# Optimization experiments

Measured on AMD Instinct MI355X. Metric: run time of the kernel, lower is better.

The kernel has to match this reference:

```python
import jax, jax.numpy as jnp
import numpy as np

NUM_LAYERS = 2
H = 1024
B = 16
L = 2048


def setup_inputs() -> dict:
    key = jax.random.key(0)
    ks = jax.random.split(key, 14)
    s = 1.0 / np.sqrt(H)
    inp = {"x": jax.random.normal(ks[0], (B, L, H), dtype=jnp.float32)}
    names = ["Wf", "Uf", "Wi", "Ui", "Wo", "Uo", "Wc", "Uc"]
    for j, n in enumerate(names):
        inp[n] = jax.random.uniform(ks[1 + j], (NUM_LAYERS, H, H), dtype=jnp.float32, minval=-s, maxval=s)
    for j, n in enumerate(["bf", "bi", "bo", "bc"]):
        inp[n] = jax.random.uniform(ks[9 + j], (NUM_LAYERS, H), dtype=jnp.float32, minval=-s, maxval=s)
    return inp


def _lstm_layer(x, W4, U4, b4, h0, c0):
    # x: [B,L,H]; W4,U4: [4H,H] packed as (f,i,o,c); b4: [4H]
    xg = jnp.einsum("blh,gh->blg", x, W4)  # [B,L,4H] input projections, one big GEMM
    xg = jnp.swapaxes(xg, 0, 1)  # [L,B,4H]

    def step(carry, xg_t):
        h, c = carry
        g = xg_t + h @ U4.T + b4  # [B,4H]
        f, i, o, cc = jnp.split(g, 4, axis=-1)
        f = jax.nn.sigmoid(f)
        i = jax.nn.sigmoid(i)
        o = jax.nn.sigmoid(o)
        c = f * c + i * jnp.tanh(cc)
        h = o * jnp.tanh(c)
        return (h, c), h

    (h_t, c_t), hs = jax.lax.scan(step, (h0, c0), xg)
    return jnp.swapaxes(hs, 0, 1), (h_t, c_t)  # [B,L,H]


def _forward(x, Wf, Uf, bf, Wi, Ui, bi, Wo, Uo, bo, Wc, Uc, bc):
    b, l, h = x.shape
    state = None
    for layer in range(NUM_LAYERS):
        W4 = jnp.concatenate([Wf[layer], Wi[layer], Wo[layer], Wc[layer]], axis=0)
        U4 = jnp.concatenate([Uf[layer], Ui[layer], Uo[layer], Uc[layer]], axis=0)
        b4 = jnp.concatenate([bf[layer], bi[layer], bo[layer], bc[layer]], axis=0)
        if state is None:
            h0 = jnp.zeros((b, h), dtype=x.dtype)
            c0 = jnp.zeros((b, h), dtype=x.dtype)
        else:
            h0, c0 = state  # source passes previous layer's final state onward
        x, state = _lstm_layer(x, W4, U4, b4, h0, c0)
        # dropout is identity in eval mode
    return x


def reference(x, Wf, Uf, bf, Wi, Ui, bi, Wo, Uo, bo, Wc, Uc, bc):
    return _forward(x, Wf, Uf, bf, Wi, Ui, bi, Wo, Uo, bo, Wc, Uc, bc)
```

## Files before the change

kernel.cpp:

```cpp
#include <hip/hip_runtime.h>


typedef _Float16 half8 __attribute__((ext_vector_type(8)));
typedef float    float4v __attribute__((ext_vector_type(4)));
typedef unsigned long long u64;

#define NBLK 256
#define NTHR 512
#define BB   16
#define LL   2048
#define HH   1024
#define KK   2048
#define NJ   4
#define NR   16
#define NSTEP 4096

#define WS_XT16   0u
#define WS_H1SEQ  67108864u
#define WS_HCUR   134217728u
#define WS_FLAGS  134283264u

struct ScanParams {
  const float* W[4];
  const float* U[4];
  const float* bias4[4];
  const _Float16* xT;
  _Float16* h1seq;
  _Float16* hcur;
  float* dout;
  unsigned* flags;
};

__global__ void prep_convert(const float* __restrict__ x, _Float16* __restrict__ xT) {
  size_t id = (size_t)blockIdx.x * blockDim.x + threadIdx.x;
  int k8 = (int)(id & (HH / 8 - 1)) * 8;
  size_t bt = id >> 7;
  int b = (int)(bt >> 11);
  int t = (int)(bt & (LL - 1));
  const float* src = x + (bt << 10) + k8;
  float4v v0 = *(const float4v*)(src);
  float4v v1 = *(const float4v*)(src + 4);
  half8 o;
  o[0] = (_Float16)v0[0]; o[1] = (_Float16)v0[1]; o[2] = (_Float16)v0[2]; o[3] = (_Float16)v0[3];
  o[4] = (_Float16)v1[0]; o[5] = (_Float16)v1[1]; o[6] = (_Float16)v1[2]; o[7] = (_Float16)v1[3];
  *(half8*)(xT + (((size_t)t * BB + b) << 10) + k8) = o;
}

__global__ void prep_init(_Float16* hcur, unsigned* flags) {
  int i = blockIdx.x * blockDim.x + threadIdx.x;
  if (i < 2 * BB * HH) hcur[i] = (_Float16)0.f;
  if (i < 1024) flags[i] = 0u;
}

__device__ __forceinline__ float sigm(float x) { return 1.f / (1.f + __expf(-x)); }
__device__ __forceinline__ float tanh_fast(float x) { return 1.f - 2.f / (1.f + __expf(2.f * x)); }

__global__ __launch_bounds__(NTHR, 2) void lstm_scan(ScanParams p) {
  __shared__ _Float16 wlds[2][NR][KK];
  __shared__ float acc_s[8][16][17];
  __shared__ float g_s[16][17];
  __shared__ float bias_s[2][NR];

  const int tid  = threadIdx.x;
  const int blk  = blockIdx.x;
  const int wv   = tid >> 6;
  const int lane = tid & 63;
  const int frow = lane & 15;
  const int kgrp = lane >> 4;

  for (int idx = tid; idx < 2 * NR * KK; idx += NTHR) {
    int l = idx >> 15;
    int r = (idx >> 11) & (NR - 1);
    int k = idx & (KK - 1);
    int q = r >> 2, jj = r & 3;
    int j = blk * NJ + jj;
    float v;
    if (k < HH) v = p.W[q][((size_t)l * HH + j) * HH + k];
    else        v = p.U[q][((size_t)l * HH + j) * HH + (k - HH)];
    unsigned bo = ((unsigned)(k * 2)) ^ ((unsigned)((r & 7) << 4));
    *(_Float16*)((char*)&wlds[l][r][0] + bo) = (_Float16)v;
  }
  if (tid < 2 * NR) {
    int l = tid >> 4, r = tid & 15;
    int q = r >> 2, jj = r & 3;
    bias_s[l][r] = p.bias4[q][l * HH + blk * NJ + jj];
  }
  float cst0 = 0.f, cst1 = 0.f, cst2 = 0.f, cst3 = 0.f;
  __syncthreads();

  unsigned* flags = p.flags;

  for (int s = 0; s < NSTEP; ++s) {
    const int l    = s >> 11;
    const int t    = s & (LL - 1);
    const int rbuf = s & 1;

    half8 aop[8], bop[8];
    if (wv < 4) {
      const _Float16* inp = (l == 0) ? p.xT : p.h1seq;
      const _Float16* abase = inp + (size_t)t * (BB * HH) + frow * HH + (wv & 3) * 256 + kgrp * 8;
#pragma unroll
      for (int kk = 0; kk < 8; ++kk)
        aop[kk] = *(const half8*)(abase + kk * 32);
    } else {
      const unsigned target = (unsigned)s;
      const int fidx = tid - 256;
      while (__hip_atomic_load(&flags[fidx], __ATOMIC_RELAXED, __HIP_MEMORY_SCOPE_AGENT) < target)
        __builtin_amdgcn_s_sleep(1);
      const u64* hb = (const u64*)(p.hcur + (size_t)rbuf * (BB * HH) + frow * HH + (wv & 3) * 256 + kgrp * 8);
#pragma unroll
      for (int kk = 0; kk < 8; ++kk) {
        union { u64 q[2]; half8 v; } u;
        u.q[0] = __hip_atomic_load(hb + kk * 8 + 0, __ATOMIC_RELAXED, __HIP_MEMORY_SCOPE_AGENT);
        u.q[1] = __hip_atomic_load(hb + kk * 8 + 1, __ATOMIC_RELAXED, __HIP_MEMORY_SCOPE_AGENT);
        aop[kk] = u.v;
      }
    }
    const int kw0 = wv * 256 + kgrp * 8;
    const char* wrow = (const char*)&wlds[l][frow][0];
#pragma unroll
    for (int kk = 0; kk < 8; ++kk) {
      unsigned bo = (unsigned)((kw0 + kk * 32) * 2) ^ ((unsigned)((frow & 7) << 4));
      bop[kk] = *(const half8*)(wrow + bo);
    }
    float4v a0 = {0.f, 0.f, 0.f, 0.f}, a1 = {0.f, 0.f, 0.f, 0.f};
#pragma unroll
    for (int kk = 0; kk < 8; kk += 2) {
      a0 = __builtin_amdgcn_mfma_f32_16x16x32_f16(aop[kk],     bop[kk],     a0, 0, 0, 0);
      a1 = __builtin_amdgcn_mfma_f32_16x16x32_f16(aop[kk + 1], bop[kk + 1], a1, 0, 0, 0);
    }
    a0 += a1;
#pragma unroll
    for (int v = 0; v < 4; ++v)
      acc_s[wv][kgrp * 4 + v][frow] = a0[v];
    __syncthreads();

    if (tid < 256) {
      int b = tid >> 4, r = tid & 15;
      float g = bias_s[l][r];
#pragma unroll
      for (int w = 0; w < 8; ++w) g += acc_s[w][b][r];
      g_s[b][r] = g;
    }
    __syncthreads();

    if (tid < 16) {
      const int b = tid;
      union { u64 q; _Float16 hv[4]; } up;
      float h0f, h1f, h2f, h3f;
      {
        float f = sigm(g_s[b][0]), i = sigm(g_s[b][4]), o = sigm(g_s[b][8]);
        cst0 = f * cst0 + i * tanh_fast(g_s[b][12]);
        h0f = o * tanh_fast(cst0); up.hv[0] = (_Float16)h0f;
      }
      {
        float f = sigm(g_s[b][1]), i = sigm(g_s[b][5]), o = sigm(g_s[b][9]);
        cst1 = f * cst1 + i * tanh_fast(g_s[b][13]);
        h1f = o * tanh_fast(cst1); up.hv[1] = (_Float16)h1f;
      }
      {
        float f = sigm(g_s[b][2]), i = sigm(g_s[b][6]), o = sigm(g_s[b][10]);
        cst2 = f * cst2 + i * tanh_fast(g_s[b][14]);
        h2f = o * tanh_fast(cst2); up.hv[2] = (_Float16)h2f;
      }
      {
        float f = sigm(g_s[b][3]), i = sigm(g_s[b][7]), o = sigm(g_s[b][11]);
        cst3 = f * cst3 + i * tanh_fast(g_s[b][15]);
        h3f = o * tanh_fast(cst3); up.hv[3] = (_Float16)h3f;
      }
      const int jg0 = blk * NJ;
      u64* hd = (u64*)(p.hcur + (size_t)(rbuf ^ 1) * (BB * HH) + b * HH + jg0);
      __hip_atomic_store(hd, up.q, __ATOMIC_RELAXED, __HIP_MEMORY_SCOPE_AGENT);
      if (l == 0) {
        u64* sd = (u64*)(p.h1seq + ((size_t)t * BB + b) * HH + jg0);
        __hip_atomic_store(sd, up.q, __ATOMIC_RELAXED, __HIP_MEMORY_SCOPE_AGENT);
      } else {
        float4v ov; ov[0] = h0f; ov[1] = h1f; ov[2] = h2f; ov[3] = h3f;
        *(float4v*)(p.dout + ((size_t)b * LL + t) * HH + jg0) = ov;
      }
    }
    if (wv == 0) {
      asm volatile("s_waitcnt vmcnt(0)" ::: "memory");
      if (lane == 0)
        __hip_atomic_store(&flags[blk], (unsigned)(s + 1), __ATOMIC_RELAXED, __HIP_MEMORY_SCOPE_AGENT);
    }
  }
}

extern "C" void kernel_launch(void* const* d_in, const int* in_sizes, int n_in,
                              void* d_out, int out_size, void* d_ws, size_t ws_size,
                              hipStream_t stream) {
  const float* x = (const float*)d_in[0];
  ScanParams sp;
  sp.W[0] = (const float*)d_in[1]; sp.U[0] = (const float*)d_in[2];
  sp.W[1] = (const float*)d_in[3]; sp.U[1] = (const float*)d_in[4];
  sp.W[2] = (const float*)d_in[5]; sp.U[2] = (const float*)d_in[6];
  sp.W[3] = (const float*)d_in[7]; sp.U[3] = (const float*)d_in[8];
  sp.bias4[0] = (const float*)d_in[9];  sp.bias4[1] = (const float*)d_in[10];
  sp.bias4[2] = (const float*)d_in[11]; sp.bias4[3] = (const float*)d_in[12];

  char* ws = (char*)d_ws;
  sp.xT    = (const _Float16*)(ws + WS_XT16);
  sp.h1seq = (_Float16*)(ws + WS_H1SEQ);
  sp.hcur  = (_Float16*)(ws + WS_HCUR);
  sp.flags = (unsigned*)(ws + WS_FLAGS);
  sp.dout  = (float*)d_out;

  prep_convert<<<16384, 256, 0, stream>>>(x, (_Float16*)(ws + WS_XT16));
  prep_init<<<128, 256, 0, stream>>>((_Float16*)(ws + WS_HCUR), (unsigned*)(ws + WS_FLAGS));
  lstm_scan<<<NBLK, NTHR, 0, stream>>>(sp);
}
```

Baseline: 30.94 ms.

## Replace flag-based grid sync with tagged hidden-state words and single-wave gate epilogue

Drops the per-block flag array and instead packs each pair of fp16 hidden values with the step tag in a 64-bit word, so consumers poll the data itself rather than first waiting on a flag and then loading. The gate epilogue is collapsed into one wavefront that reduces partial sums, applies the LSTM cell and uses lane shuffles to pack outputs, which removes one __syncthreads and the g_s staging. The accumulator buffer is double-buffered by step parity so the next step's writes do not race the reduction. This aims to shorten the latency of each serial timestep, at the cost of doubling the bytes polled and reissuing all 32 loads whenever any tag is stale.

```diff
diff --git a/kernel.cpp b/kernel.cpp
--- a/kernel.cpp
+++ b/kernel.cpp
@@ -4,6 +4,7 @@
 typedef _Float16 half8 __attribute__((ext_vector_type(8)));
 typedef float    float4v __attribute__((ext_vector_type(4)));
 typedef unsigned long long u64;
+typedef unsigned u32;
 
 #define NBLK 256
 #define NTHR 512
@@ -17,8 +18,7 @@
 
 #define WS_XT16   0u
 #define WS_H1SEQ  67108864u
-#define WS_HCUR   134217728u
-#define WS_FLAGS  134283264u
+#define WS_HPUB   134217728u
 
 struct ScanParams {
   const float* W[4];
@@ -26,9 +26,8 @@
   const float* bias4[4];
   const _Float16* xT;
   _Float16* h1seq;
-  _Float16* hcur;
+  u64* hpub;
   float* dout;
-  unsigned* flags;
 };
 
 __global__ void prep_convert(const float* __restrict__ x, _Float16* __restrict__ xT) {
@@ -46,10 +45,9 @@
   *(half8*)(xT + (((size_t)t * BB + b) << 10) + k8) = o;
 }
 
-__global__ void prep_init(_Float16* hcur, unsigned* flags) {
+__global__ void prep_init(u64* hpub) {
   int i = blockIdx.x * blockDim.x + threadIdx.x;
-  if (i < 2 * BB * HH) hcur[i] = (_Float16)0.f;
-  if (i < 1024) flags[i] = 0u;
+  if (i < 2 * BB * 256 * 2) hpub[i] = 0ull;
 }
 
 __device__ __forceinline__ float sigm(float x) { return 1.f / (1.f + __expf(-x)); }
@@ -57,8 +55,7 @@
 
 __global__ __launch_bounds__(NTHR, 2) void lstm_scan(ScanParams p) {
   __shared__ _Float16 wlds[2][NR][KK];
-  __shared__ float acc_s[8][16][17];
-  __shared__ float g_s[16][17];
+  __shared__ float acc_s[2][8][16][17];
   __shared__ float bias_s[2][NR];
 
   const int tid  = threadIdx.x;
@@ -82,42 +79,55 @@
   }
   if (tid < 2 * NR) {
     int l = tid >> 4, r = tid & 15;
-    int q = r >> 2, jj = r & 3;
-    bias_s[l][r] = p.bias4[q][l * HH + blk * NJ + jj];
+    bias_s[l][r] = p.bias4[r >> 2][l * HH + blk * NJ + (r & 3)];
   }
-  float cst0 = 0.f, cst1 = 0.f, cst2 = 0.f, cst3 = 0.f;
+  float cst = 0.f;
   __syncthreads();
 
-  unsigned* flags = p.flags;
-
   for (int s = 0; s < NSTEP; ++s) {
-    const int l    = s >> 11;
-    const int t    = s & (LL - 1);
-    const int rbuf = s & 1;
-
-    half8 aop[8], bop[8];
+    const int l   = s >> 11;
+    const int t   = s & (LL - 1);
+    const int par = s & 1;
+
+    half8 aop[8];
     if (wv < 4) {
       const _Float16* inp = (l == 0) ? p.xT : p.h1seq;
-      const _Float16* abase = inp + (size_t)t * (BB * HH) + frow * HH + (wv & 3) * 256 + kgrp * 8;
+      const _Float16* ab = inp + (size_t)t * (BB * HH) + frow * HH + wv * 256 + kgrp * 8;
 #pragma unroll
       for (int kk = 0; kk < 8; ++kk)
-        aop[kk] = *(const half8*)(abase + kk * 32);
+        aop[kk] = *(const half8*)(ab + kk * 32);
     } else {
-      const unsigned target = (unsigned)s;
-      const int fidx = tid - 256;
-      while (__hip_atomic_load(&flags[fidx], __ATOMIC_RELAXED, __HIP_MEMORY_SCOPE_AGENT) < target)
-        __builtin_amdgcn_s_sleep(1);
-      const u64* hb = (const u64*)(p.hcur + (size_t)rbuf * (BB * HH) + frow * HH + (wv & 3) * 256 + kgrp * 8);
+      const int hw = wv - 4;
+      const u64* hp = p.hpub + (size_t)par * (BB * 256 * 2);
+      const u32 want = (u32)s;
+      const int qb = frow * 512 + hw * 128 + kgrp * 4;
+      u64 q[32];
+      bool ok = false;
+      while (!ok) {
+#pragma unroll
+        for (int kk = 0; kk < 8; ++kk) {
+#pragma unroll
+          for (int j = 0; j < 4; ++j)
+            q[kk * 4 + j] = __hip_atomic_load(hp + qb + kk * 16 + j,
+                                              __ATOMIC_RELAXED, __HIP_MEMORY_SCOPE_AGENT);
+        }
+        ok = true;
+#pragma unroll
+        for (int i = 0; i < 32; ++i) ok &= ((u32)(q[i] >> 32) == want);
+        if (!ok) __builtin_amdgcn_s_sleep(1);
+      }
 #pragma unroll
       for (int kk = 0; kk < 8; ++kk) {
-        union { u64 q[2]; half8 v; } u;
-        u.q[0] = __hip_atomic_load(hb + kk * 8 + 0, __ATOMIC_RELAXED, __HIP_MEMORY_SCOPE_AGENT);
-        u.q[1] = __hip_atomic_load(hb + kk * 8 + 1, __ATOMIC_RELAXED, __HIP_MEMORY_SCOPE_AGENT);
+        union { u32 w[4]; half8 v; } u;
+        u.w[0] = (u32)q[kk * 4 + 0]; u.w[1] = (u32)q[kk * 4 + 1];
+        u.w[2] = (u32)q[kk * 4 + 2]; u.w[3] = (u32)q[kk * 4 + 3];
         aop[kk] = u.v;
       }
     }
+
     const int kw0 = wv * 256 + kgrp * 8;
     const char* wrow = (const char*)&wlds[l][frow][0];
+    half8 bop[8];
 #pragma unroll
     for (int kk = 0; kk < 8; ++kk) {
       unsigned bo = (unsigned)((kw0 + kk * 32) * 2) ^ ((unsigned)((frow & 7) << 4));
@@ -132,57 +142,48 @@
     a0 += a1;
 #pragma unroll
     for (int v = 0; v < 4; ++v)
-      acc_s[wv][kgrp * 4 + v][frow] = a0[v];
+      acc_s[par][wv][kgrp * 4 + v][frow] = a0[v];
     __syncthreads();
 
-    if (tid < 256) {
-      int b = tid >> 4, r = tid & 15;
-      float g = bias_s[l][r];
-#pragma unroll
-      for (int w = 0; w < 8; ++w) g += acc_s[w][b][r];
-      g_s[b][r] = g;
-    }
-    __syncthreads();
-
-    if (tid < 16) {
-      const int b = tid;
-      union { u64 q; _Float16 hv[4]; } up;
-      float h0f, h1f, h2f, h3f;
-      {
-        float f = sigm(g_s[b][0]), i = sigm(g_s[b][4]), o = sigm(g_s[b][8]);
-        cst0 = f * cst0 + i * tanh_fast(g_s[b][12]);
-        h0f = o * tanh_fast(cst0); up.hv[0] = (_Float16)h0f;
-      }
-      {
-        float f = sigm(g_s[b][1]), i = sigm(g_s[b][5]), o = sigm(g_s[b][9]);
-        cst1 = f * cst1 + i * tanh_fast(g_s[b][13]);
-        h1f = o * tanh_fast(cst1); up.hv[1] = (_Float16)h1f;
-      }
-      {
-        float f = sigm(g_s[b][2]), i = sigm(g_s[b][6]), o = sigm(g_s[b][10]);
-        cst2 = f * cst2 + i * tanh_fast(g_s[b][14]);
-        h2f = o * tanh_fast(cst2); up.hv[2] = (_Float16)h2f;
-      }
-      {
-        float f = sigm(g_s[b][3]), i = sigm(g_s[b][7]), o = sigm(g_s[b][11]);
-        cst3 = f * cst3 + i * tanh_fast(g_s[b][15]);
-        h3f = o * tanh_fast(cst3); up.hv[3] = (_Float16)h3f;
-      }
-      const int jg0 = blk * NJ;
-      u64* hd = (u64*)(p.hcur + (size_t)(rbuf ^ 1) * (BB * HH) + b * HH + jg0);
-      __hip_atomic_store(hd, up.q, __ATOMIC_RELAXED, __HIP_MEMORY_SCOPE_AGENT);
-      if (l == 0) {
-        u64* sd = (u64*)(p.h1seq + ((size_t)t * BB + b) * HH + jg0);
-        __hip_atomic_store(sd, up.q, __ATOMIC_RELAXED, __HIP_MEMORY_SCOPE_AGENT);
-      } else {
-        float4v ov; ov[0] = h0f; ov[1] = h1f; ov[2] = h2f; ov[3] = h3f;
-        *(float4v*)(p.dout + ((size_t)b * LL + t) * HH + jg0) = ov;
-      }
-    }
     if (wv == 0) {
-      asm volatile("s_waitcnt vmcnt(0)" ::: "memory");
-      if (lane == 0)
-        __hip_atomic_store(&flags[blk], (unsigned)(s + 1), __ATOMIC_RELAXED, __HIP_MEMORY_SCOPE_AGENT);
+      const int b = lane >> 2, jj = lane & 3;
+      float g0 = bias_s[l][jj],      g1 = bias_s[l][4 + jj];
+      float g2 = bias_s[l][8 + jj],  g3 = bias_s[l][12 + jj];
+#pragma unroll
+      for (int w = 0; w < 8; ++w) {
+        g0 += acc_s[par][w][b][jj];
+        g1 += acc_s[par][w][b][4 + jj];
+        g2 += acc_s[par][w][b][8 + jj];
+        g3 += acc_s[par][w][b][12 + jj];
+      }
+      float f = sigm(g0), i = sigm(g1), o = sigm(g2), cc = tanh_fast(g3);
+      cst = f * cst + i * cc;
+      float hf = o * tanh_fast(cst);
+
+      union { _Float16 h; unsigned short us; } cv; cv.h = (_Float16)hf;
+      u32 hu = cv.us;
+      u32 v1 = __shfl_xor(hu, 1);
+      u32 v2 = __shfl_xor(hu, 2);
+      u32 v3 = __shfl_xor(v1, 2);
+      float f1 = __shfl_xor(hf, 1);
+      float f2 = __shfl_xor(hf, 2);
+      float f3 = __shfl_xor(f1, 2);
+      if (jj == 0) {
+        u32 pair01 = hu | (v1 << 16);
+        u32 pair23 = v2 | (v3 << 16);
+        u64 tagw = ((u64)(u32)(s + 1)) << 32;
+        u64* dst = p.hpub + (size_t)((s + 1) & 1) * (BB * 256 * 2) + b * 512 + blk * 2;
+        __hip_atomic_store(dst + 0, (u64)pair01 | tagw, __ATOMIC_RELAXED, __HIP_MEMORY_SCOPE_AGENT);
+        __hip_atomic_store(dst + 1, (u64)pair23 | tagw, __ATOMIC_RELAXED, __HIP_MEMORY_SCOPE_AGENT);
+        if (l == 0) {
+          u64 hq = (u64)pair01 | ((u64)pair23 << 32);
+          __hip_atomic_store((u64*)(p.h1seq + ((size_t)t * BB + b) * HH + blk * 4), hq,
+                             __ATOMIC_RELAXED, __HIP_MEMORY_SCOPE_AGENT);
+        } else {
+          float4v ov; ov[0] = hf; ov[1] = f1; ov[2] = f2; ov[3] = f3;
+          *(float4v*)(p.dout + ((size_t)b * LL + t) * HH + blk * 4) = ov;
+        }
+      }
     }
   }
 }
@@ -202,11 +203,10 @@
   char* ws = (char*)d_ws;
   sp.xT    = (const _Float16*)(ws + WS_XT16);
   sp.h1seq = (_Float16*)(ws + WS_H1SEQ);
-  sp.hcur  = (_Float16*)(ws + WS_HCUR);
-  sp.flags = (unsigned*)(ws + WS_FLAGS);
+  sp.hpub  = (u64*)(ws + WS_HPUB);
   sp.dout  = (float*)d_out;
 
   prep_convert<<<16384, 256, 0, stream>>>(x, (_Float16*)(ws + WS_XT16));
-  prep_init<<<128, 256, 0, stream>>>((_Float16*)(ws + WS_HCUR), (unsigned*)(ws + WS_FLAGS));
+  prep_init<<<64, 256, 0, stream>>>((u64*)(ws + WS_HPUB));
   lstm_scan<<<NBLK, NTHR, 0, stream>>>(sp);
 }
```

Result: slower. 55.77 ms (+80.2%).
